# Optimization experiments

Hardware: AMD Instinct MI355X
Metric: run time of the kernel (lower is better)

Reference implementation:

```python
import jax, jax.numpy as jnp
import numpy as np

N_HE = 6_000_000
N_V = 1_000_000
D = 32

def setup_inputs() -> dict:
    key = jax.random.key(0)
    k1, k2 = jax.random.split(key)
    x = jax.random.normal(k1, (N_HE, D), dtype=jnp.float32)
    vertex_ids = jax.random.randint(k2, (N_HE,), 0, N_V, dtype=jnp.int32)
    return {"x": x, "vertex_ids": vertex_ids, "n_vertices": N_V}

def reference(x, vertex_ids, n_vertices):
    # scatter-add half-edge features into their from-vertex bins
    out = jax.ops.segment_sum(x, vertex_ids, num_segments=n_vertices)  # [V, D]
    # valence = number of outgoing half-edges per vertex
    valence = jax.ops.segment_sum(jnp.ones((x.shape[0],), dtype=x.dtype),
                                  vertex_ids, num_segments=n_vertices)  # [V]
    valence = jnp.maximum(valence, 1.0)  # guard isolated vertices
    return out / valence[:, None]
```

## Files before the change

kernel.cpp:

```cpp
#include <hip/hip_runtime.h>

#define DFEAT 32
#define SCAN_CHUNK 1024
#define VPG 4


__global__ void he2v_hist(const int* __restrict__ ids,
                          int* __restrict__ counts, int n_he) {
    long tid = (long)blockIdx.x * blockDim.x + threadIdx.x;
    long stride = (long)gridDim.x * blockDim.x;
    long n4 = n_he >> 2;
    for (long t = tid; t < n4; t += stride) {
        int4 w = ((const int4*)ids)[t];
        atomicAdd(&counts[w.x], 1);
        atomicAdd(&counts[w.y], 1);
        atomicAdd(&counts[w.z], 1);
        atomicAdd(&counts[w.w], 1);
    }
    int rem = n_he & 3;
    if (tid < rem) atomicAdd(&counts[ids[(n4 << 2) + tid]], 1);
}

__global__ void he2v_chunk_reduce(const int* __restrict__ counts,
                                  int* __restrict__ chunkSums, int n_v) {
    int b = blockIdx.x, t = threadIdx.x;
    int idx = b * SCAN_CHUNK + t * 4;
    int s = 0;
    if (idx + 3 < n_v) {
        int4 c = *(const int4*)(counts + idx);
        s = c.x + c.y + c.z + c.w;
    } else {
        for (int j = 0; j < 4; ++j)
            if (idx + j < n_v) s += counts[idx + j];
    }
    for (int off = 32; off; off >>= 1) s += __shfl_down(s, off, 64);
    __shared__ int ws[4];
    if ((t & 63) == 0) ws[t >> 6] = s;
    __syncthreads();
    if (t == 0) chunkSums[b] = ws[0] + ws[1] + ws[2] + ws[3];
}

__global__ void he2v_scan_chunks(int* __restrict__ cs, int n) {
    __shared__ int buf[1024];
    __shared__ int carry_s;
    int t = threadIdx.x;
    if (t == 0) carry_s = 0;
    __syncthreads();
    for (int base = 0; base < n; base += 1024) {
        int i = base + t;
        int v = (i < n) ? cs[i] : 0;
        buf[t] = v;
        __syncthreads();
        for (int off = 1; off < 1024; off <<= 1) {
            int tv = (t >= off) ? buf[t - off] : 0;
            __syncthreads();
            buf[t] += tv;
            __syncthreads();
        }
        int incl = buf[t];
        int carry = carry_s;
        __syncthreads();
        if (i < n) cs[i] = carry + incl - v;
        if (t == 1023) carry_s = carry + incl;
        __syncthreads();
    }
}

__global__ void he2v_scan_apply(const int* __restrict__ counts,
                                const int* __restrict__ chunkExcl,
                                int* __restrict__ cursor, int n_v) {
    int b = blockIdx.x, t = threadIdx.x;
    int idx = b * SCAN_CHUNK + t * 4;
    int c0 = 0, c1 = 0, c2 = 0, c3 = 0;
    if (idx + 3 < n_v) {
        int4 c = *(const int4*)(counts + idx);
        c0 = c.x; c1 = c.y; c2 = c.z; c3 = c.w;
    } else {
        if (idx     < n_v) c0 = counts[idx];
        if (idx + 1 < n_v) c1 = counts[idx + 1];
        if (idx + 2 < n_v) c2 = counts[idx + 2];
        if (idx + 3 < n_v) c3 = counts[idx + 3];
    }
    int s = c0 + c1 + c2 + c3;
    __shared__ int sb[256];
    sb[t] = s;
    __syncthreads();
    for (int off = 1; off < 256; off <<= 1) {
        int v = (t >= off) ? sb[t - off] : 0;
        __syncthreads();
        sb[t] += v;
        __syncthreads();
    }
    int base = chunkExcl[b] + sb[t] - s;
    if (idx     < n_v) cursor[idx]     = base; base += c0;
    if (idx + 1 < n_v) cursor[idx + 1] = base; base += c1;
    if (idx + 2 < n_v) cursor[idx + 2] = base; base += c2;
    if (idx + 3 < n_v) cursor[idx + 3] = base;
}

__global__ void he2v_perm_build(const int* __restrict__ ids,
                                int* __restrict__ cursor,
                                int* __restrict__ perm, int n_he) {
    long tid = (long)blockIdx.x * blockDim.x + threadIdx.x;
    long stride = (long)gridDim.x * blockDim.x;
    long n4 = n_he >> 2;
    for (long t = tid; t < n4; t += stride) {
        int4 w = ((const int4*)ids)[t];
        int i0 = (int)(t << 2);
        int p;
        p = atomicAdd(&cursor[w.x], 1); perm[p] = i0;
        p = atomicAdd(&cursor[w.y], 1); perm[p] = i0 + 1;
        p = atomicAdd(&cursor[w.z], 1); perm[p] = i0 + 2;
        p = atomicAdd(&cursor[w.w], 1); perm[p] = i0 + 3;
    }
    int rem = n_he & 3;
    if (tid < rem) {
        int i = (int)(n4 << 2) + (int)tid;
        int p = atomicAdd(&cursor[ids[i]], 1);
        perm[p] = i;
    }
}

__global__ void he2v_gather(const float* __restrict__ x,
                            const int* __restrict__ counts,
                            const int* __restrict__ cursor,
                            const int* __restrict__ perm,
                            float* __restrict__ out, int n_v) {
    long tid = (long)blockIdx.x * blockDim.x + threadIdx.x;
    long group = tid >> 3;
    int q = (int)(tid & 7);
    long v0 = group * VPG;
    if (v0 >= n_v) return;
    const float4* x4 = (const float4*)x;
    float4* out4 = (float4*)out;
    for (int vv = 0; vv < VPG; ++vv) {
        long v = v0 + vv;
        if (v >= n_v) break;
        int c = counts[v];
        int base = cursor[v] - c;
        float4 acc = make_float4(0.f, 0.f, 0.f, 0.f);
        for (int k = 0; k < c; ++k) {
            int he = perm[base + k];
            float4 xv = x4[(long)he * 8 + q];
            acc.x += xv.x; acc.y += xv.y; acc.z += xv.z; acc.w += xv.w;
        }
        float inv = 1.0f / (float)(c > 0 ? c : 1);
        float4 o;
        o.x = acc.x * inv; o.y = acc.y * inv;
        o.z = acc.z * inv; o.w = acc.w * inv;
        out4[v * 8 + q] = o;
    }
}

__global__ void he2v_scatter(const float* __restrict__ x,
                             const int* __restrict__ ids,
                             float* __restrict__ out,
                             float* __restrict__ val,
                             int n_he) {
    long tid = (long)blockIdx.x * blockDim.x + threadIdx.x;
    long stride = (long)gridDim.x * blockDim.x;
    long total = (long)n_he * 8;
    for (long t = tid; t < total; t += stride) {
        int row = (int)(t >> 3);
        int q   = (int)(t & 7);
        int v   = ids[row];
        float4 xv = ((const float4*)x)[(long)row * 8 + q];
        float* dst = out + (long)v * DFEAT + q * 4;
        atomicAdd(dst + 0, xv.x);
        atomicAdd(dst + 1, xv.y);
        atomicAdd(dst + 2, xv.z);
        atomicAdd(dst + 3, xv.w);
        if (q == 0) atomicAdd(val + v, 1.0f);
    }
}

__global__ void he2v_divide(float* __restrict__ out,
                            const float* __restrict__ val,
                            int n_v) {
    long tid = (long)blockIdx.x * blockDim.x + threadIdx.x;
    long total = (long)n_v * 8;
    if (tid >= total) return;
    int v = (int)(tid >> 3);
    float s = val[v];
    if (s < 1.0f) s = 1.0f;
    float4 o = ((float4*)out)[tid];
    o.x /= s; o.y /= s; o.z /= s; o.w /= s;
    ((float4*)out)[tid] = o;
}

extern "C" void kernel_launch(void* const* d_in, const int* in_sizes, int n_in,
                              void* d_out, int out_size, void* d_ws, size_t ws_size,
                              hipStream_t stream) {
    const float* x  = (const float*)d_in[0];
    const int* ids  = (const int*)d_in[1];
    int n_he = in_sizes[0] / DFEAT;
    int n_v  = out_size / DFEAT;
    float* out = (float*)d_out;

    int nchunks = (n_v + SCAN_CHUNK - 1) / SCAN_CHUNK;
    int ncp = (nchunks + 3) & ~3;
    size_t need = ((size_t)2 * n_v + (size_t)ncp + (size_t)n_he) * sizeof(int);

    if (ws_size >= need) {
        int* counts    = (int*)d_ws;
        int* chunkSums = counts + n_v;
        int* cursor    = chunkSums + ncp;
        int* perm      = cursor + n_v;

        hipMemsetAsync(counts, 0, (size_t)n_v * sizeof(int), stream);
        he2v_hist<<<2048, 256, 0, stream>>>(ids, counts, n_he);
        he2v_chunk_reduce<<<nchunks, 256, 0, stream>>>(counts, chunkSums, n_v);
        he2v_scan_chunks<<<1, 1024, 0, stream>>>(chunkSums, nchunks);
        he2v_scan_apply<<<nchunks, 256, 0, stream>>>(counts, chunkSums, cursor, n_v);
        he2v_perm_build<<<4096, 256, 0, stream>>>(ids, cursor, perm, n_he);

        long groups = ((long)n_v + VPG - 1) / VPG;
        long threads = groups * 8;
        int blocks = (int)((threads + 255) / 256);
        he2v_gather<<<blocks, 256, 0, stream>>>(x, counts, cursor, perm, out, n_v);
    } else {
        float* val = (float*)d_ws;
        hipMemsetAsync(out, 0, (size_t)out_size * sizeof(float), stream);
        hipMemsetAsync(val, 0, (size_t)n_v * sizeof(float), stream);
        he2v_scatter<<<8192, 256, 0, stream>>>(x, ids, out, val, n_he);
        long total = (long)n_v * 8;
        int blocks = (int)((total + 255) / 256);
        he2v_divide<<<blocks, 256, 0, stream>>>(out, val, n_v);
    }
}
```

Before: 1.832 ms.

## Physically reorder features into a sorted buffer before the segment gather

Replaces the permutation-index build with a reorder kernel that copies each half-edge's 128-byte feature row into a vertex-sorted buffer. The gather then reads contiguous rows instead of chasing perm indices into random rows of x. This costs an extra full write and read of the feature array (about 768MB of workspace) in exchange for coalesced reads in the gather. It falls back to the old perm path when the workspace is too small.

```diff
diff --git a/kernel.cpp b/kernel.cpp
--- a/kernel.cpp
+++ b/kernel.cpp
@@ -96,6 +96,54 @@
     if (idx + 1 < n_v) cursor[idx + 1] = base; base += c1;
     if (idx + 2 < n_v) cursor[idx + 2] = base; base += c2;
     if (idx + 3 < n_v) cursor[idx + 3] = base;
+}
+
+
+__global__ void he2v_reorder(const float* __restrict__ x,
+                             const int* __restrict__ ids,
+                             int* __restrict__ cursor,
+                             float4* __restrict__ sorted,
+                             int n_he) {
+    long tid = (long)blockIdx.x * blockDim.x + threadIdx.x;
+    long gstride = ((long)gridDim.x * blockDim.x) >> 3;
+    long group = tid >> 3;
+    int q = (int)(tid & 7);
+    const float4* x4 = (const float4*)x;
+    for (long row = group; row < n_he; row += gstride) {
+        float4 xv = x4[row * 8 + q];
+        int p = 0;
+        if (q == 0) p = atomicAdd(&cursor[ids[row]], 1);
+        p = __shfl(p, 0, 8);
+        sorted[(long)p * 8 + q] = xv;
+    }
+}
+
+__global__ void he2v_gather_sorted(const float4* __restrict__ sorted,
+                                   const int* __restrict__ counts,
+                                   const int* __restrict__ cursor,
+                                   float* __restrict__ out, int n_v) {
+    long tid = (long)blockIdx.x * blockDim.x + threadIdx.x;
+    long group = tid >> 3;
+    int q = (int)(tid & 7);
+    long v0 = group * VPG;
+    if (v0 >= n_v) return;
+    float4* out4 = (float4*)out;
+    for (int vv = 0; vv < VPG; ++vv) {
+        long v = v0 + vv;
+        if (v >= n_v) break;
+        int c = counts[v];
+        long base = (long)(cursor[v] - c);
+        float4 acc = make_float4(0.f, 0.f, 0.f, 0.f);
+        for (int k = 0; k < c; ++k) {
+            float4 xv = sorted[(base + k) * 8 + q];
+            acc.x += xv.x; acc.y += xv.y; acc.z += xv.z; acc.w += xv.w;
+        }
+        float inv = 1.0f / (float)(c > 0 ? c : 1);
+        float4 o;
+        o.x = acc.x * inv; o.y = acc.y * inv;
+        o.z = acc.z * inv; o.w = acc.w * inv;
+        out4[v * 8 + q] = o;
+    }
 }
 
 __global__ void he2v_perm_build(const int* __restrict__ ids,
@@ -199,25 +247,38 @@
 
     int nchunks = (n_v + SCAN_CHUNK - 1) / SCAN_CHUNK;
     int ncp = (nchunks + 3) & ~3;
-    size_t need = ((size_t)2 * n_v + (size_t)ncp + (size_t)n_he) * sizeof(int);
-
-    if (ws_size >= need) {
+
+    size_t headInts = ((size_t)2 * n_v + (size_t)ncp + 3) & ~(size_t)3;
+    size_t need_full = headInts * sizeof(int)
+                     + (size_t)n_he * DFEAT * sizeof(float);
+    size_t need_perm = ((size_t)2 * n_v + (size_t)ncp + (size_t)n_he) * sizeof(int);
+
+    if (ws_size >= need_full || ws_size >= need_perm) {
         int* counts    = (int*)d_ws;
         int* chunkSums = counts + n_v;
         int* cursor    = chunkSums + ncp;
-        int* perm      = cursor + n_v;
 
         hipMemsetAsync(counts, 0, (size_t)n_v * sizeof(int), stream);
         he2v_hist<<<2048, 256, 0, stream>>>(ids, counts, n_he);
         he2v_chunk_reduce<<<nchunks, 256, 0, stream>>>(counts, chunkSums, n_v);
         he2v_scan_chunks<<<1, 1024, 0, stream>>>(chunkSums, nchunks);
         he2v_scan_apply<<<nchunks, 256, 0, stream>>>(counts, chunkSums, cursor, n_v);
-        he2v_perm_build<<<4096, 256, 0, stream>>>(ids, cursor, perm, n_he);
 
         long groups = ((long)n_v + VPG - 1) / VPG;
         long threads = groups * 8;
-        int blocks = (int)((threads + 255) / 256);
-        he2v_gather<<<blocks, 256, 0, stream>>>(x, counts, cursor, perm, out, n_v);
+        int gblocks = (int)((threads + 255) / 256);
+
+        if (ws_size >= need_full) {
+            float4* sorted = (float4*)((int*)d_ws + headInts);
+            he2v_reorder<<<8192, 256, 0, stream>>>(x, ids, cursor, sorted, n_he);
+            he2v_gather_sorted<<<gblocks, 256, 0, stream>>>(sorted, counts, cursor,
+                                                            out, n_v);
+        } else {
+            int* perm = cursor + n_v;
+            he2v_perm_build<<<4096, 256, 0, stream>>>(ids, cursor, perm, n_he);
+            he2v_gather<<<gblocks, 256, 0, stream>>>(x, counts, cursor, perm,
+                                                     out, n_v);
+        }
     } else {
         float* val = (float*)d_ws;
         hipMemsetAsync(out, 0, (size_t)out_size * sizeof(float), stream);
```

New measurement: 1.991 ms. 8.7% more time.
